# Optimization experiments

Hardware: AMD Instinct MI355X
Metric: run time of the kernel (lower is better)

The kernel has to match this reference:

```python
import jax, jax.numpy as jnp
import numpy as np

B, N, OBS = 512, 64, 256
H1, H2 = 4, 4
D = 128            # embed/key dim (d_k_1 = d_k_2 = 128)
O1 = D // H1       # 32, per-head value dim stage 1
O2 = D // H2       # 32, per-head value dim stage 2
IN2 = O1 * H1      # 128, input dim to stage 2
FOUT = 16          # final_output_dim


def setup_inputs() -> dict:
    key = jax.random.key(0)
    ks = jax.random.split(key, 22)
    g = lambda k, shp: (jax.random.normal(k, shp, dtype=jnp.float32) * 0.05)
    inp = {
        "states": jax.random.normal(ks[0], (B, N, OBS), dtype=jnp.float32),
        # stage 1 per-head params, stacked over heads
        "E1_w": g(ks[1], (H1, D, OBS)), "E1_b": g(ks[2], (H1, D)),
        "K1_w": g(ks[3], (H1, D, D)),   "K1_b": g(ks[4], (H1, D)),
        "Q1_w": g(ks[5], (H1, D, D)),   "Q1_b": g(ks[6], (H1, D)),
        "V1_w": g(ks[7], (H1, O1, D)),  "V1_b": g(ks[8], (H1, O1)),
        # stage 2 per-head params
        "E2_w": g(ks[9], (H2, D, IN2)), "E2_b": g(ks[10], (H2, D)),
        "K2_w": g(ks[11], (H2, D, D)),  "K2_b": g(ks[12], (H2, D)),
        "Q2_w": g(ks[13], (H2, D, D)),  "Q2_b": g(ks[14], (H2, D)),
        "V2_w": g(ks[15], (H2, O2, D)), "V2_b": g(ks[16], (H2, O2)),
        # final MLP policy head
        "F1_w": g(ks[17], (64, O2 * H2)), "F1_b": g(ks[18], (64,)),
        "F2_w": g(ks[19], (FOUT, 64)),    "F2_b": g(ks[20], (FOUT,)),
    }
    return inp


def _attn_block(x, Ew, Eb, Kw, Kb, Qw, Qb, Vw, Vb, d_k):
    # x: [B,N,I]; all head loops batched via leading head axis h
    se = jax.nn.leaky_relu(jnp.einsum('bni,hdi->hbnd', x, Ew) + Eb[:, None, None, :])  # [h,B,N,D]
    k = jnp.einsum('hbnd,hed->hbne', se, Kw) + Kb[:, None, None, :]
    q = jnp.einsum('hbnd,hed->hbne', se, Qw) + Qb[:, None, None, :]
    w = jax.nn.softmax(jnp.einsum('hbne,hbme->hbnm', q, k) / jnp.sqrt(jnp.float32(d_k)), axis=-1)  # [h,B,N,N]
    v = jax.nn.leaky_relu(jnp.einsum('hbnd,hod->hbno', se, Vw) + Vb[:, None, None, :])  # [h,B,N,O]
    att = jnp.einsum('hbnm,hbmo->hbno', w, v)
    h, b, n, o = att.shape
    return jnp.transpose(att, (1, 2, 0, 3)).reshape(b, n, h * o), w


def reference(states, E1_w, E1_b, K1_w, K1_b, Q1_w, Q1_b, V1_w, V1_b,
              E2_w, E2_b, K2_w, K2_b, Q2_w, Q2_b, V2_w, V2_b,
              F1_w, F1_b, F2_w, F2_b):
    x1, w1 = _attn_block(states, E1_w, E1_b, K1_w, K1_b, Q1_w, Q1_b, V1_w, V1_b, D)
    x2, w2 = _attn_block(x1, E2_w, E2_b, K2_w, K2_b, Q2_w, Q2_b, V2_w, V2_b, D)
    h = jax.nn.leaky_relu(jnp.einsum('bnf,of->bno', x2, F1_w) + F1_b)
    policy = jax.nn.softmax(jnp.einsum('bno,po->bnp', h, F2_w) + F2_b, axis=-1)
    return policy, w1, w2
```

## Files before the change

### kernel.cpp

```cpp
#include <hip/hip_runtime.h>

typedef __attribute__((ext_vector_type(8))) short short8;
typedef __attribute__((ext_vector_type(4))) short short4v;
typedef __attribute__((ext_vector_type(4))) float f32x4;

#define MFMA(a, b, c) __builtin_amdgcn_mfma_f32_16x16x32_bf16((a), (b), (c), 0, 0, 0)

__device__ __forceinline__ short f2bf(float f) {
    union { float f; unsigned u; } v; v.f = f;
    unsigned r = v.u + 0x7fffu + ((v.u >> 16) & 1u);
    return (short)(r >> 16);
}
__device__ __forceinline__ float bf2f(short s) {
    union { unsigned u; float f; } v; v.u = ((unsigned)(unsigned short)s) << 16; return v.f;
}

struct PrepArgs {
    const float* csrc[6]; int cend[6];
    const float* K1w; const float* Q1w; const float* Q1b;
    const float* K2w; const float* Q2w; const float* Q2b;
};

__global__ __launch_bounds__(256) void prep_kernel(PrepArgs a, short* __restrict__ dstW,
                                                   short* __restrict__ M1, short* __restrict__ M2) {
    const int blk = blockIdx.x, t = threadIdx.x;
    if (blk < 233) {
        int i4 = blk * 256 + t;
        int seg = 0;
#pragma unroll
        for (int s = 0; s < 5; s++) seg += (i4 >= a.cend[s]) ? 1 : 0;
        int base = (seg == 0) ? 0 : a.cend[seg - 1];
        float4 v = ((const float4*)a.csrc[seg])[i4 - base];
        short4v o; o.x = f2bf(v.x); o.y = f2bf(v.y); o.z = f2bf(v.z); o.w = f2bf(v.w);
        *(short4v*)(dstW + (size_t)i4 * 4) = o;
    } else {
        int mi = blk - 233;
        int mat = mi / 9, rg = mi % 9;
        int s = mat >> 2, h = mat & 3;
        const float* Kw = s ? a.K2w : a.K1w;
        const float* Qw = s ? a.Q2w : a.Q1w;
        const float* Qb = s ? a.Q2b : a.Q1b;
        short* Mt = (s ? M2 : M1) + h * 144 * 128;
        int r  = rg * 16 + (t >> 4);
        int d0 = (t & 15) * 8;
        float acc[8];
#pragma unroll
        for (int j = 0; j < 8; j++) acc[j] = 0.f;
        const float* kw = Kw + (size_t)h * 16384;
        if (r < 128) {
            const float* qw = Qw + (size_t)h * 16384;
            for (int e = 0; e < 128; e++) {
                float kv = kw[e * 128 + r];
                const float* q = qw + e * 128 + d0;
#pragma unroll
                for (int j = 0; j < 8; j++) acc[j] = fmaf(kv, q[j], acc[j]);
            }
        } else if (r == 128) {
            const float* qb = Qb + h * 128;
            for (int e = 0; e < 128; e++) {
                float qv = qb[e];
                const float* kk = kw + e * 128 + d0;
#pragma unroll
                for (int j = 0; j < 8; j++) acc[j] = fmaf(qv, kk[j], acc[j]);
            }
        }
#pragma unroll
        for (int j = 0; j < 8; j++) Mt[r * 128 + d0 + j] = f2bf(acc[j]);
    }
}

#define SE_LD  136
#define T_LD   136
#define VT_LD  72
#define W_LD   72
#define W32_LD 68
#define R1     8704
#define R2     17408
#define D2OFF  19712
#define SMEM_SHORTS 19840

template<int IN, bool XF32>
__global__ __launch_bounds__(256, 4) void attn_stage_kernel(
    const void* __restrict__ xin,
    const short* __restrict__ Ew, const float* __restrict__ Eb,
    const short* __restrict__ Mt,
    const short* __restrict__ Vw, const float* __restrict__ Vb,
    float* __restrict__ w_out,
    short* __restrict__ x_out)
{
    __shared__ short sm[SMEM_SHORTS];
    const int tid  = threadIdx.x;
    const int b    = blockIdx.x & 511;
    const int h    = blockIdx.x >> 9;
    const int wv   = tid >> 6;
    const int lane = tid & 63;
    const int quad = lane >> 4;
    const int l16  = lane & 15;
    constexpr int NK1   = IN / 32;
    constexpr int XLD   = IN + 8;
    constexpr int XBASE = XF32 ? 0 : R1;

    if constexpr (XF32) {
        const float* xb = (const float*)xin + (size_t)b * 64 * IN;
#pragma unroll
        for (int r = 0; r < 16; r++) {
            int f4 = tid + 256 * r;
            int row = f4 >> 6, c4 = (f4 & 63) * 4;
            float4 v = ((const float4*)xb)[f4];
            short4v o; o.x = f2bf(v.x); o.y = f2bf(v.y); o.z = f2bf(v.z); o.w = f2bf(v.w);
            *(short4v*)&sm[row * XLD + c4] = o;
        }
    } else {
        const short* xb = (const short*)xin + (size_t)b * 64 * IN;
#pragma unroll
        for (int r = 0; r < 4; r++) {
            int f8 = tid + 256 * r;
            int row = f8 >> 4, c8 = (f8 & 15) * 8;
            short8 v = *(const short8*)(xb + (size_t)f8 * 8);
            *(short8*)&sm[XBASE + row * 136 + c8] = v;
        }
    }

    short8 ebf[NK1 * 2];
    {
        const short* ewh = Ew + (size_t)h * 128 * IN;
#pragma unroll
        for (int k0i = 0; k0i < NK1; k0i++)
#pragma unroll
            for (int j = 0; j < 2; j++)
                ebf[k0i * 2 + j] = *(const short8*)(ewh + (size_t)(wv * 32 + j * 16 + l16) * IN + k0i * 32 + quad * 8);
    }
    __syncthreads();

    short8 mbf[8], xbf[4], vbf[4];

    {
        f32x4 acc[4][2];
#pragma unroll
        for (int j = 0; j < 2; j++) {
            float bv = Eb[h * 128 + wv * 32 + j * 16 + l16];
            f32x4 c = {bv, bv, bv, bv};
#pragma unroll
            for (int i = 0; i < 4; i++) acc[i][j] = c;
        }
#pragma unroll
        for (int k0i = 0; k0i < NK1; k0i++) {
            short8 a[4];
#pragma unroll
            for (int i = 0; i < 4; i++)
                a[i] = *(const short8*)&sm[XBASE + (i * 16 + l16) * XLD + k0i * 32 + quad * 8];
#pragma unroll
            for (int i = 0; i < 4; i++)
#pragma unroll
                for (int j = 0; j < 2; j++)
                    acc[i][j] = MFMA(a[i], ebf[k0i * 2 + j], acc[i][j]);
        }
        {
            const short* mth = Mt + (size_t)h * 144 * 128;
#pragma unroll
            for (int k0i = 0; k0i < 4; k0i++) {
#pragma unroll
                for (int j = 0; j < 2; j++)
                    mbf[k0i * 2 + j] = *(const short8*)(mth + (size_t)(wv * 32 + j * 16 + l16) * 128 + k0i * 32 + quad * 8);
                xbf[k0i] = *(const short8*)(mth + (size_t)(128 + l16) * 128 + k0i * 32 + quad * 8);
                vbf[k0i] = *(const short8*)(Vw + (size_t)h * 32 * 128 + (size_t)(((wv >> 1) * 16) + l16) * 128 + k0i * 32 + quad * 8);
            }
        }
        if constexpr (XF32) __syncthreads();
#pragma unroll
        for (int i = 0; i < 4; i++)
#pragma unroll
            for (int j = 0; j < 2; j++)
#pragma unroll
                for (int r = 0; r < 4; r++) {
                    float v = acc[i][j][r];
                    v = (v >= 0.f) ? v : 0.01f * v;
                    sm[(i * 16 + quad * 4 + r) * SE_LD + wv * 32 + j * 16 + l16] = f2bf(v);
                }
    }
    __syncthreads();

    {
        f32x4 tacc[4][2], dacc[4];
#pragma unroll
        for (int i = 0; i < 4; i++) {
#pragma unroll
            for (int j = 0; j < 2; j++) tacc[i][j] = (f32x4){0.f, 0.f, 0.f, 0.f};
            dacc[i] = (f32x4){0.f, 0.f, 0.f, 0.f};
        }
#pragma unroll
        for (int k0i = 0; k0i < 4; k0i++) {
            short8 a[4];
#pragma unroll
            for (int i = 0; i < 4; i++)
                a[i] = *(const short8*)&sm[(i * 16 + l16) * SE_LD + k0i * 32 + quad * 8];
#pragma unroll
            for (int i = 0; i < 4; i++)
#pragma unroll
                for (int j = 0; j < 2; j++)
                    tacc[i][j] = MFMA(a[i], mbf[k0i * 2 + j], tacc[i][j]);
            if (wv == 0) {
#pragma unroll
                for (int i = 0; i < 4; i++) dacc[i] = MFMA(a[i], xbf[k0i], dacc[i]);
            }
        }
#pragma unroll
        for (int i = 0; i < 4; i++)
#pragma unroll
            for (int j = 0; j < 2; j++)
#pragma unroll
                for (int r = 0; r < 4; r++)
                    sm[R1 + (i * 16 + quad * 4 + r) * T_LD + wv * 32 + j * 16 + l16] = f2bf(tacc[i][j][r]);
        if (wv == 0 && l16 == 0) {
            float* d2f = (float*)&sm[D2OFF];
#pragma unroll
            for (int i = 0; i < 4; i++)
#pragma unroll
                for (int r = 0; r < 4; r++)
                    d2f[i * 16 + quad * 4 + r] = dacc[i][r];
        }
        const int n0v = (wv >> 1) * 16, mrow = (wv & 1) * 32;
        float vb = Vb[h * 32 + n0v + l16];
        f32x4 vacc[2]; vacc[0] = (f32x4){vb, vb, vb, vb}; vacc[1] = vacc[0];
#pragma unroll
        for (int k0i = 0; k0i < 4; k0i++) {
            short8 a0 = *(const short8*)&sm[(mrow + l16) * SE_LD + k0i * 32 + quad * 8];
            short8 a1 = *(const short8*)&sm[(mrow + 16 + l16) * SE_LD + k0i * 32 + quad * 8];
            vacc[0] = MFMA(a0, vbf[k0i], vacc[0]);
            vacc[1] = MFMA(a1, vbf[k0i], vacc[1]);
        }
#pragma unroll
        for (int i = 0; i < 2; i++)
#pragma unroll
            for (int r = 0; r < 4; r++) {
                float v = vacc[i][r];
                v = (v >= 0.f) ? v : 0.01f * v;
                sm[R2 + (n0v + l16) * VT_LD + mrow + i * 16 + quad * 4 + r] = f2bf(v);
            }
    }
    __syncthreads();

    float d2v[4];
    {
        const float* d2f = (const float*)&sm[D2OFF];
#pragma unroll
        for (int jj = 0; jj < 4; jj++) d2v[jj] = d2f[jj * 16 + l16];
    }
    f32x4 lacc[4];
#pragma unroll
    for (int jj = 0; jj < 4; jj++) lacc[jj] = (f32x4){0.f, 0.f, 0.f, 0.f};
#pragma unroll
    for (int k0 = 0; k0 < 128; k0 += 32) {
        short8 a = *(const short8*)&sm[R1 + (wv * 16 + l16) * T_LD + k0 + quad * 8];
#pragma unroll
        for (int jj = 0; jj < 4; jj++) {
            short8 b8 = *(const short8*)&sm[(jj * 16 + l16) * SE_LD + k0 + quad * 8];
            lacc[jj] = MFMA(a, b8, lacc[jj]);
        }
    }
    __syncthreads();

    {
        const float scale = 0.08838834764831845f;
        float* w32 = (float*)sm;
#pragma unroll
        for (int jj = 0; jj < 4; jj++)
#pragma unroll
            for (int r = 0; r < 4; r++) lacc[jj][r] += d2v[jj];
        float mx[4], inv[4];
#pragma unroll
        for (int r = 0; r < 4; r++) {
            float m = lacc[0][r];
#pragma unroll
            for (int jj = 1; jj < 4; jj++) m = fmaxf(m, lacc[jj][r]);
#pragma unroll
            for (int s = 1; s < 16; s <<= 1) m = fmaxf(m, __shfl_xor(m, s, 16));
            mx[r] = m;
        }
        float sum[4] = {0.f, 0.f, 0.f, 0.f};
#pragma unroll
        for (int jj = 0; jj < 4; jj++)
#pragma unroll
            for (int r = 0; r < 4; r++) {
                float e = __expf((lacc[jj][r] - mx[r]) * scale);
                lacc[jj][r] = e; sum[r] += e;
            }
#pragma unroll
        for (int r = 0; r < 4; r++) {
#pragma unroll
            for (int s = 1; s < 16; s <<= 1) sum[r] += __shfl_xor(sum[r], s, 16);
            inv[r] = 1.0f / sum[r];
        }
#pragma unroll
        for (int r = 0; r < 4; r++) {
            int row = wv * 16 + quad * 4 + r;
#pragma unroll
            for (int jj = 0; jj < 4; jj++) {
                float wval = lacc[jj][r] * inv[r];
                w32[row * W32_LD + jj * 16 + l16] = wval;
                sm[R1 + row * W_LD + jj * 16 + l16] = f2bf(wval);
            }
        }
    }
    __syncthreads();

    {
        const float* w32 = (const float*)sm;
        float* wbase = w_out + ((size_t)(h * 512 + b)) * 64 * 64;
#pragma unroll
        for (int s = 0; s < 4; s++) {
            int idx = tid + 256 * s;
            int row = idx >> 4, c4 = (idx & 15) * 4;
            f32x4 v = *(const f32x4*)&w32[row * W32_LD + c4];
            __builtin_nontemporal_store(v, (f32x4*)(wbase + idx * 4));
        }
    }

    {
        f32x4 aacc[2]; aacc[0] = (f32x4){0.f, 0.f, 0.f, 0.f}; aacc[1] = aacc[0];
#pragma unroll
        for (int k0 = 0; k0 < 64; k0 += 32) {
            short8 a = *(const short8*)&sm[R1 + (wv * 16 + l16) * W_LD + k0 + quad * 8];
#pragma unroll
            for (int j = 0; j < 2; j++) {
                short8 b8 = *(const short8*)&sm[R2 + (j * 16 + l16) * VT_LD + k0 + quad * 8];
                aacc[j] = MFMA(a, b8, aacc[j]);
            }
        }
        short* xob = x_out + (size_t)b * 64 * 128;
#pragma unroll
        for (int j = 0; j < 2; j++)
#pragma unroll
            for (int r = 0; r < 4; r++)
                xob[(size_t)(wv * 16 + quad * 4 + r) * 128 + h * 32 + j * 16 + l16] = f2bf(aacc[j][r]);
    }
}

#define H_LD 72
__global__ __launch_bounds__(256)
void final_mlp_mfma_kernel(const short* __restrict__ x2,
                           const short* __restrict__ F1wb,
                           const float* __restrict__ F1b,
                           const short* __restrict__ F2wb,
                           const float* __restrict__ F2b,
                           float* __restrict__ policy)
{
    __shared__ short hsm[4][16 * H_LD];
    const int tid  = threadIdx.x;
    const int wv   = tid >> 6;
    const int lane = tid & 63;
    const int quad = lane >> 4;
    const int l16  = lane & 15;
    const int rowbase = blockIdx.x * 64 + wv * 16;

    short8 a[4];
    const short* xrow = x2 + (size_t)(rowbase + l16) * 128;
#pragma unroll
    for (int k = 0; k < 4; k++) a[k] = *(const short8*)(xrow + k * 32 + quad * 8);
    f32x4 acc[4];
#pragma unroll
    for (int j = 0; j < 4; j++) { float bv = F1b[j * 16 + l16]; acc[j] = (f32x4){bv, bv, bv, bv}; }
#pragma unroll
    for (int k = 0; k < 4; k++)
#pragma unroll
        for (int j = 0; j < 4; j++) {
            short8 b8 = *(const short8*)(F1wb + (size_t)(j * 16 + l16) * 128 + k * 32 + quad * 8);
            acc[j] = MFMA(a[k], b8, acc[j]);
        }
    short* hh = &hsm[wv][0];
#pragma unroll
    for (int j = 0; j < 4; j++)
#pragma unroll
        for (int r = 0; r < 4; r++) {
            float v = acc[j][r];
            v = (v >= 0.f) ? v : 0.01f * v;
            hh[(quad * 4 + r) * H_LD + j * 16 + l16] = f2bf(v);
        }
    __syncthreads();

    f32x4 lg;
    { float bv = F2b[l16]; lg = (f32x4){bv, bv, bv, bv}; }
#pragma unroll
    for (int k = 0; k < 2; k++) {
        short8 a2 = *(const short8*)(hh + l16 * H_LD + k * 32 + quad * 8);
        short8 b8 = *(const short8*)(F2wb + (size_t)l16 * 64 + k * 32 + quad * 8);
        lg = MFMA(a2, b8, lg);
    }
#pragma unroll
    for (int r = 0; r < 4; r++) {
        float m = lg[r];
        m = fmaxf(m, __shfl_xor(m, 1, 16));
        m = fmaxf(m, __shfl_xor(m, 2, 16));
        m = fmaxf(m, __shfl_xor(m, 4, 16));
        m = fmaxf(m, __shfl_xor(m, 8, 16));
        float e = __expf(lg[r] - m);
        float s = e;
        s += __shfl_xor(s, 1, 16);
        s += __shfl_xor(s, 2, 16);
        s += __shfl_xor(s, 4, 16);
        s += __shfl_xor(s, 8, 16);
        policy[(size_t)(rowbase + quad * 4 + r) * 16 + l16] = e / s;
    }
}

extern "C" void kernel_launch(void* const* d_in, const int* in_sizes, int n_in,
                              void* d_out, int out_size, void* d_ws, size_t ws_size,
                              hipStream_t stream) {
    const float* states = (const float*)d_in[0];
    const float* E1w = (const float*)d_in[1];  const float* E1b = (const float*)d_in[2];
    const float* K1w = (const float*)d_in[3];
    const float* Q1w = (const float*)d_in[5];  const float* Q1b = (const float*)d_in[6];
    const float* V1w = (const float*)d_in[7];  const float* V1b = (const float*)d_in[8];
    const float* E2w = (const float*)d_in[9];  const float* E2b = (const float*)d_in[10];
    const float* K2w = (const float*)d_in[11];
    const float* Q2w = (const float*)d_in[13]; const float* Q2b = (const float*)d_in[14];
    const float* V2w = (const float*)d_in[15]; const float* V2b = (const float*)d_in[16];
    const float* F1w = (const float*)d_in[17]; const float* F1b = (const float*)d_in[18];
    const float* F2w = (const float*)d_in[19]; const float* F2b = (const float*)d_in[20];

    float* out    = (float*)d_out;
    float* policy = out;
    float* w1     = out + 512 * 64 * 16;
    float* w2     = w1 + 4 * 512 * 64 * 64;

    short* wsb = (short*)d_ws;
    short* x1b = wsb;
    short* x2b = wsb + 4194304;
    short* wts = wsb + 8388608;
    short* wE1 = wts;            short* wV1 = wts + 131072;
    short* wE2 = wts + 147456;   short* wV2 = wts + 212992;
    short* wF1 = wts + 229376;   short* wF2 = wts + 237568;
    short* M1  = wts + 238592;   short* M2  = M1 + 73728;

    PrepArgs pa;
    pa.csrc[0] = E1w; pa.csrc[1] = V1w; pa.csrc[2] = E2w;
    pa.csrc[3] = V2w; pa.csrc[4] = F1w; pa.csrc[5] = F2w;
    pa.cend[0] = 32768; pa.cend[1] = 36864; pa.cend[2] = 53248;
    pa.cend[3] = 57344; pa.cend[4] = 59392; pa.cend[5] = 59648;
    pa.K1w = K1w; pa.Q1w = Q1w; pa.Q1b = Q1b;
    pa.K2w = K2w; pa.Q2w = Q2w; pa.Q2b = Q2b;
    prep_kernel<<<305, 256, 0, stream>>>(pa, wts, M1, M2);

    attn_stage_kernel<256, true><<<2048, 256, 0, stream>>>(
        (const void*)states, wE1, E1b, M1, wV1, V1b, w1, x1b);
    attn_stage_kernel<128, false><<<2048, 256, 0, stream>>>(
        (const void*)x1b, wE2, E2b, M2, wV2, V2b, w2, x2b);
    final_mlp_mfma_kernel<<<512, 256, 0, stream>>>(x2b, wF1, F1b, wF2, F2b, policy);
}
```

Measured before the change: 230.2 us.

## Pre-convert states to bf16 once and store attention outputs in per-head strips

When the workspace is large enough, the prep kernel now converts `states` to bf16 alongside the weights. Stage 1 then reads that bf16 copy instead of reading and converting fp32 inputs in every one of the four head blocks. The per-stage outputs move to a head-major strip layout (head × batch × row × 32), so each head block writes contiguous rows and later kernels read strips. Prep block order is swapped and its inner loops get unroll pragmas. The cost is an extra 16MB workspace buffer and a larger prep launch, with a fallback path kept for small workspaces.

```diff
diff --git a/kernel.cpp b/kernel.cpp
--- a/kernel.cpp
+++ b/kernel.cpp
@@ -11,12 +11,9 @@
     unsigned r = v.u + 0x7fffu + ((v.u >> 16) & 1u);
     return (short)(r >> 16);
 }
-__device__ __forceinline__ float bf2f(short s) {
-    union { unsigned u; float f; } v; v.u = ((unsigned)(unsigned short)s) << 16; return v.f;
-}
 
 struct PrepArgs {
-    const float* csrc[6]; int cend[6];
+    const float* csrc[7]; int cend[7];
     const float* K1w; const float* Q1w; const float* Q1b;
     const float* K2w; const float* Q2w; const float* Q2b;
 };
@@ -24,18 +21,8 @@
 __global__ __launch_bounds__(256) void prep_kernel(PrepArgs a, short* __restrict__ dstW,
                                                    short* __restrict__ M1, short* __restrict__ M2) {
     const int blk = blockIdx.x, t = threadIdx.x;
-    if (blk < 233) {
-        int i4 = blk * 256 + t;
-        int seg = 0;
-#pragma unroll
-        for (int s = 0; s < 5; s++) seg += (i4 >= a.cend[s]) ? 1 : 0;
-        int base = (seg == 0) ? 0 : a.cend[seg - 1];
-        float4 v = ((const float4*)a.csrc[seg])[i4 - base];
-        short4v o; o.x = f2bf(v.x); o.y = f2bf(v.y); o.z = f2bf(v.z); o.w = f2bf(v.w);
-        *(short4v*)(dstW + (size_t)i4 * 4) = o;
-    } else {
-        int mi = blk - 233;
-        int mat = mi / 9, rg = mi % 9;
+    if (blk < 72) {
+        int mat = blk / 9, rg = blk % 9;
         int s = mat >> 2, h = mat & 3;
         const float* Kw = s ? a.K2w : a.K1w;
         const float* Qw = s ? a.Q2w : a.Q1w;
@@ -49,6 +36,7 @@
         const float* kw = Kw + (size_t)h * 16384;
         if (r < 128) {
             const float* qw = Qw + (size_t)h * 16384;
+#pragma unroll 4
             for (int e = 0; e < 128; e++) {
                 float kv = kw[e * 128 + r];
                 const float* q = qw + e * 128 + d0;
@@ -57,6 +45,7 @@
             }
         } else if (r == 128) {
             const float* qb = Qb + h * 128;
+#pragma unroll 4
             for (int e = 0; e < 128; e++) {
                 float qv = qb[e];
                 const float* kk = kw + e * 128 + d0;
@@ -66,6 +55,15 @@
         }
 #pragma unroll
         for (int j = 0; j < 8; j++) Mt[r * 128 + d0 + j] = f2bf(acc[j]);
+    } else {
+        int i4 = (blk - 72) * 256 + t;
+        int seg = 0;
+#pragma unroll
+        for (int s = 0; s < 6; s++) seg += (i4 >= a.cend[s]) ? 1 : 0;
+        int base = (seg == 0) ? 0 : a.cend[seg - 1];
+        float4 v = ((const float4*)a.csrc[seg])[i4 - base];
+        short4v o; o.x = f2bf(v.x); o.y = f2bf(v.y); o.z = f2bf(v.z); o.w = f2bf(v.w);
+        *(short4v*)(dstW + (size_t)i4 * 4) = o;
     }
 }
 
@@ -78,6 +76,7 @@
 #define R2     17408
 #define D2OFF  19712
 #define SMEM_SHORTS 19840
+#define HSTRIDE 1048576
 
 template<int IN, bool XF32>
 __global__ __launch_bounds__(256, 4) void attn_stage_kernel(
@@ -98,7 +97,7 @@
     const int l16  = lane & 15;
     constexpr int NK1   = IN / 32;
     constexpr int XLD   = IN + 8;
-    constexpr int XBASE = XF32 ? 0 : R1;
+    constexpr int XBASE = (IN == 256) ? 0 : R1;
 
     if constexpr (XF32) {
         const float* xb = (const float*)xin + (size_t)b * 64 * IN;
@@ -110,14 +109,24 @@
             short4v o; o.x = f2bf(v.x); o.y = f2bf(v.y); o.z = f2bf(v.z); o.w = f2bf(v.w);
             *(short4v*)&sm[row * XLD + c4] = o;
         }
+    } else if constexpr (IN == 256) {
+        const short* xb = (const short*)xin + (size_t)b * 64 * 256;
+#pragma unroll
+        for (int r = 0; r < 8; r++) {
+            int f8 = tid + 256 * r;
+            int row = f8 >> 5, c8 = (f8 & 31) * 8;
+            short8 v = *(const short8*)(xb + (size_t)f8 * 8);
+            *(short8*)&sm[row * XLD + c8] = v;
+        }
     } else {
-        const short* xb = (const short*)xin + (size_t)b * 64 * IN;
+        const short* xb = (const short*)xin;
 #pragma unroll
         for (int r = 0; r < 4; r++) {
             int f8 = tid + 256 * r;
             int row = f8 >> 4, c8 = (f8 & 15) * 8;
-            short8 v = *(const short8*)(xb + (size_t)f8 * 8);
-            *(short8*)&sm[XBASE + row * 136 + c8] = v;
+            int strip = c8 >> 5, col = c8 & 31;
+            short8 v = *(const short8*)(xb + (size_t)strip * HSTRIDE + ((size_t)b * 64 + row) * 32 + col);
+            *(short8*)&sm[R1 + row * 136 + c8] = v;
         }
     }
 
@@ -166,7 +175,7 @@
                 vbf[k0i] = *(const short8*)(Vw + (size_t)h * 32 * 128 + (size_t)(((wv >> 1) * 16) + l16) * 128 + k0i * 32 + quad * 8);
             }
         }
-        if constexpr (XF32) __syncthreads();
+        if constexpr (IN == 256) __syncthreads();
 #pragma unroll
         for (int i = 0; i < 4; i++)
 #pragma unroll
@@ -327,12 +336,12 @@
                 aacc[j] = MFMA(a, b8, aacc[j]);
             }
         }
-        short* xob = x_out + (size_t)b * 64 * 128;
+        short* xob = x_out + (size_t)h * HSTRIDE + (size_t)b * 64 * 32;
 #pragma unroll
         for (int j = 0; j < 2; j++)
 #pragma unroll
             for (int r = 0; r < 4; r++)
-                xob[(size_t)(wv * 16 + quad * 4 + r) * 128 + h * 32 + j * 16 + l16] = f2bf(aacc[j][r]);
+                xob[(wv * 16 + quad * 4 + r) * 32 + j * 16 + l16] = f2bf(aacc[j][r]);
     }
 }
 
@@ -354,9 +363,9 @@
     const int rowbase = blockIdx.x * 64 + wv * 16;
 
     short8 a[4];
-    const short* xrow = x2 + (size_t)(rowbase + l16) * 128;
-#pragma unroll
-    for (int k = 0; k < 4; k++) a[k] = *(const short8*)(xrow + k * 32 + quad * 8);
+#pragma unroll
+    for (int k = 0; k < 4; k++)
+        a[k] = *(const short8*)(x2 + (size_t)k * HSTRIDE + (size_t)(rowbase + l16) * 32 + quad * 8);
     f32x4 acc[4];
 #pragma unroll
     for (int j = 0; j < 4; j++) { float bv = F1b[j * 16 + l16]; acc[j] = (f32x4){bv, bv, bv, bv}; }
@@ -424,26 +433,54 @@
     float* w2     = w1 + 4 * 512 * 64 * 64;
 
     short* wsb = (short*)d_ws;
-    short* x1b = wsb;
-    short* x2b = wsb + 4194304;
-    short* wts = wsb + 8388608;
-    short* wE1 = wts;            short* wV1 = wts + 131072;
-    short* wE2 = wts + 147456;   short* wV2 = wts + 212992;
-    short* wF1 = wts + 229376;   short* wF2 = wts + 237568;
-    short* M1  = wts + 238592;   short* M2  = M1 + 73728;
-
     PrepArgs pa;
-    pa.csrc[0] = E1w; pa.csrc[1] = V1w; pa.csrc[2] = E2w;
-    pa.csrc[3] = V2w; pa.csrc[4] = F1w; pa.csrc[5] = F2w;
-    pa.cend[0] = 32768; pa.cend[1] = 36864; pa.cend[2] = 53248;
-    pa.cend[3] = 57344; pa.cend[4] = 59392; pa.cend[5] = 59648;
     pa.K1w = K1w; pa.Q1w = Q1w; pa.Q1b = Q1b;
     pa.K2w = K2w; pa.Q2w = Q2w; pa.Q2b = Q2b;
-    prep_kernel<<<305, 256, 0, stream>>>(pa, wts, M1, M2);
-
-    attn_stage_kernel<256, true><<<2048, 256, 0, stream>>>(
-        (const void*)states, wE1, E1b, M1, wV1, V1b, w1, x1b);
-    attn_stage_kernel<128, false><<<2048, 256, 0, stream>>>(
-        (const void*)x1b, wE2, E2b, M2, wV2, V2b, w2, x2b);
-    final_mlp_mfma_kernel<<<512, 256, 0, stream>>>(x2b, wF1, F1b, wF2, F2b, policy);
+
+    const size_t need = (size_t)12968960 * 2;
+
+    if (ws_size >= need) {
+        short* x1b = wsb;
+        short* xsb = wsb + 4194304;
+        short* x2b = xsb;
+        short* wts = wsb + 12582912;
+        short* wE1 = wts;            short* wV1 = wts + 131072;
+        short* wE2 = wts + 147456;   short* wV2 = wts + 212992;
+        short* wF1 = wts + 229376;   short* wF2 = wts + 237568;
+        short* M1  = wts + 238592;   short* M2  = M1 + 73728;
+
+        pa.csrc[0] = states; pa.csrc[1] = E1w; pa.csrc[2] = V1w; pa.csrc[3] = E2w;
+        pa.csrc[4] = V2w;    pa.csrc[5] = F1w; pa.csrc[6] = F2w;
+        pa.cend[0] = 2097152; pa.cend[1] = 2129920; pa.cend[2] = 2134016;
+        pa.cend[3] = 2150400; pa.cend[4] = 2154496; pa.cend[5] = 2156544;
+        pa.cend[6] = 2156800;
+        prep_kernel<<<72 + 8425, 256, 0, stream>>>(pa, xsb, M1, M2);
+
+        attn_stage_kernel<256, false><<<2048, 256, 0, stream>>>(
+            (const void*)xsb, wE1, E1b, M1, wV1, V1b, w1, x1b);
+        attn_stage_kernel<128, false><<<2048, 256, 0, stream>>>(
+            (const void*)x1b, wE2, E2b, M2, wV2, V2b, w2, x2b);
+        final_mlp_mfma_kernel<<<512, 256, 0, stream>>>(x2b, wF1, F1b, wF2, F2b, policy);
+    } else {
+        short* x1b = wsb;
+        short* x2b = wsb + 4194304;
+        short* wts = wsb + 8388608;
+        short* wE1 = wts;            short* wV1 = wts + 131072;
+        short* wE2 = wts + 147456;   short* wV2 = wts + 212992;
+        short* wF1 = wts + 229376;   short* wF2 = wts + 237568;
+        short* M1  = wts + 238592;   short* M2  = M1 + 73728;
+
+        pa.csrc[0] = E1w; pa.csrc[1] = V1w; pa.csrc[2] = E2w;
+        pa.csrc[3] = V2w; pa.csrc[4] = F1w; pa.csrc[5] = F2w; pa.csrc[6] = F2w;
+        pa.cend[0] = 32768; pa.cend[1] = 36864; pa.cend[2] = 53248;
+        pa.cend[3] = 57344; pa.cend[4] = 59392; pa.cend[5] = 59648;
+        pa.cend[6] = 59648;
+        prep_kernel<<<72 + 233, 256, 0, stream>>>(pa, wts, M1, M2);
+
+        attn_stage_kernel<256, true><<<2048, 256, 0, stream>>>(
+            (const void*)states, wE1, E1b, M1, wV1, V1b, w1, x1b);
+        attn_stage_kernel<128, false><<<2048, 256, 0, stream>>>(
+            (const void*)x1b, wE2, E2b, M2, wV2, V2b, w2, x2b);
+        final_mlp_mfma_kernel<<<512, 256, 0, stream>>>(x2b, wF1, F1b, wF2, F2b, policy);
+    }
 }
```

Result: no change. 233.9 us (+1.6%).
